# Kernel optimization log

Hardware: AMD Instinct MI355X
Metric: run time of the kernel (lower is better)

Reference implementation:

```python
import jax, jax.numpy as jnp
import numpy as np

H = 16  # num_heads
E = 1024  # embed_dim
HD = E // H  # head_dim = 64


def setup_inputs() -> dict:
    key = jax.random.key(0)
    k1, k2, k3 = jax.random.split(key, 3)
    n, bs = 2048, 2
    # xavier-uniform-ish scale for weights
    seq = jax.random.normal(k1, (n, bs, E), dtype=jnp.float32)
    w_qkv = jax.random.normal(k2, (3 * E, E), dtype=jnp.float32) * (2.0 / (E + 3 * E)) ** 0.5
    b_qkv = jnp.zeros((3 * E,), dtype=jnp.float32)
    w_out = jax.random.normal(k3, (E, E), dtype=jnp.float32) * (1.0 / E) ** 0.5
    b_out = jnp.zeros((E,), dtype=jnp.float32)
    return {"seq": seq, "w_qkv": w_qkv, "b_qkv": b_qkv, "w_out": w_out, "b_out": b_out}


def reference(seq, w_qkv, b_qkv, w_out, b_out):
    n, bs, _ = seq.shape
    # fused QKV projection: [n, bs, 3E]
    qkv = jnp.einsum('nbe,fe->nbf', seq, w_qkv) + b_qkv
    # reshape to [n, bs, 3, H, HD] then split -> q,k,v each [n, bs, H, HD]
    qkv = qkv.reshape(n, bs, 3, H, HD)
    q = qkv[:, :, 0] / jnp.asarray(HD, seq.dtype) ** 0.5
    k = qkv[:, :, 1]
    v = qkv[:, :, 2]
    # scores [bs, H, n, n] -- explicitly materialized as in the original
    attn = jnp.einsum('qbhd,kbhd->bhqk', q, k)
    attn = jax.nn.softmax(attn, axis=-1)
    # weighted values back to [n, bs, H, HD] -> [n, bs, E]
    out = jnp.einsum('bhqk,kbhd->qbhd', attn, v).reshape(n, bs, E)
    out = jnp.einsum('nbe,fe->nbf', out, w_out) + b_out
    return out
```

## Files before the change

### kernel.cpp

```cpp
#include <hip/hip_runtime.h>

typedef unsigned short u16;
typedef unsigned int u32;
typedef __bf16 bf16_8 __attribute__((ext_vector_type(8)));
typedef short s16x8 __attribute__((ext_vector_type(8)));
typedef short s16x4 __attribute__((ext_vector_type(4)));
typedef float f32x4 __attribute__((ext_vector_type(4)));

#define NQ 2048
#define BSZ 2
#define EDIM 1024
#define NH 16
#define HDIM 64
#define MROWS (NQ * BSZ)
#define F3 (3 * EDIM)

__device__ __forceinline__ float bf2f(u16 u) {
  u32 x = ((u32)u) << 16;
  return __builtin_bit_cast(float, x);
}
__device__ __forceinline__ u16 f2bf(float f) {
  u32 x = __builtin_bit_cast(u32, f);
  x += 0x7fff + ((x >> 16) & 1);
  return (u16)(x >> 16);
}
__device__ __forceinline__ void gload16(const u16* g, u16* l) {
  __builtin_amdgcn_global_load_lds(
      (const __attribute__((address_space(1))) void*)g,
      (__attribute__((address_space(3))) void*)l, 16, 0, 0);
}

__global__ __launch_bounds__(256) void cvt_f32_bf16(
    const float* __restrict__ in, u16* __restrict__ out, int n) {
  int i = (blockIdx.x * 256 + threadIdx.x) * 4;
  const int stride = gridDim.x * 256 * 4;
  for (; i < n; i += stride) {
    f32x4 v = *(const f32x4*)&in[i];
    s16x4 o;
    o[0] = (short)f2bf(v[0]);
    o[1] = (short)f2bf(v[1]);
    o[2] = (short)f2bf(v[2]);
    o[3] = (short)f2bf(v[3]);
    *(s16x4*)&out[i] = o;
  }
}

__global__ __launch_bounds__(512, 2) void gemm_qkv(
    const u16* __restrict__ A, const u16* __restrict__ B,
    const float* __restrict__ bias,
    u16* __restrict__ out0, u16* __restrict__ out1, u16* __restrict__ out2) {
  constexpr int K = EDIM;
  __shared__ u16 As[2][256 * 32];
  __shared__ u16 Bs[2][192 * 32];
  const int tid = threadIdx.x;
  const int wid = tid >> 6, lane = tid & 63;
  const int wr = wid >> 2, wc = wid & 3;
  const int row0 = blockIdx.y * 256, col0 = blockIdx.x * 192;
  const int g = lane >> 4, l15 = lane & 15;
  const int lr = tid >> 2, lc8 = (tid & 3) * 8;

  auto STAGE = [&](int buf, int kb) {
    gload16(&A[(size_t)(row0 + lr) * K + kb + lc8], &As[buf][wid * 512]);
    gload16(&A[(size_t)(row0 + 128 + lr) * K + kb + lc8],
            &As[buf][4096 + wid * 512]);
    gload16(&B[(size_t)(col0 + lr) * K + kb + lc8], &Bs[buf][wid * 512]);
    if (tid < 256)
      gload16(&B[(size_t)(col0 + 128 + lr) * K + kb + lc8],
              &Bs[buf][4096 + wid * 512]);
  };

  f32x4 acc[8][3];
#pragma unroll
  for (int m = 0; m < 8; ++m)
#pragma unroll
    for (int n = 0; n < 3; ++n) acc[m][n] = f32x4{0.f, 0.f, 0.f, 0.f};

  STAGE(0, 0);
  __syncthreads();
  int cur = 0;
  for (int t = 0; t < 32; ++t) {
    if (t < 31) STAGE(cur ^ 1, (t + 1) * 32);
    bf16_8 af[8], bf[3];
#pragma unroll
    for (int m = 0; m < 8; ++m)
      af[m] = __builtin_bit_cast(
          bf16_8, *(const s16x8*)&As[cur][(wr * 128 + m * 16 + l15) * 32 + g * 8]);
#pragma unroll
    for (int n = 0; n < 3; ++n)
      bf[n] = __builtin_bit_cast(
          bf16_8, *(const s16x8*)&Bs[cur][(wc * 48 + n * 16 + l15) * 32 + g * 8]);
#pragma unroll
    for (int m = 0; m < 8; ++m)
#pragma unroll
      for (int n = 0; n < 3; ++n)
        acc[m][n] = __builtin_amdgcn_mfma_f32_16x16x32_bf16(af[m], bf[n],
                                                            acc[m][n], 0, 0, 0);
    __syncthreads();
    cur ^= 1;
  }

  const int orow = row0 + wr * 128;
  const int ocol = col0 + wc * 48;
#pragma unroll
  for (int m = 0; m < 8; ++m) {
#pragma unroll
    for (int n = 0; n < 3; ++n) {
      const int f = ocol + n * 16 + l15;
      const float bv = bias[f];
#pragma unroll
      for (int j = 0; j < 4; ++j) {
        const int r = orow + m * 16 + g * 4 + j;
        const float v = acc[m][n][j] + bv;
        const int part = f >> 10, e = f & 1023;
        const int h = e >> 6, d = e & 63;
        const int nq = r >> 1, b = r & 1;
        const int bh = b * NH + h;
        if (part == 0)
          out0[((size_t)bh * NQ + nq) * HDIM + d] = f2bf(v * 0.125f);
        else if (part == 1)
          out1[((size_t)bh * NQ + nq) * HDIM + d] = f2bf(v);
        else
          out2[((size_t)bh * HDIM + d) * NQ + nq] = f2bf(v);
      }
    }
  }
}

__global__ __launch_bounds__(256) void gemm_out(
    const u16* __restrict__ A, const u16* __restrict__ B,
    const float* __restrict__ bias, float* __restrict__ outf) {
  constexpr int K = EDIM;
  __shared__ u16 As[2][128 * 32];
  __shared__ u16 Bs[2][128 * 32];
  const int tid = threadIdx.x;
  const int wid = tid >> 6, lane = tid & 63;
  const int wm = wid >> 1, wn = wid & 1;
  const int row0 = blockIdx.y * 128, col0 = blockIdx.x * 128;
  const int g = lane >> 4, l15 = lane & 15;
  const int lr = tid >> 2, lc8 = (tid & 3) * 8;

  auto STAGE = [&](int buf, int kb) {
#pragma unroll
    for (int s = 0; s < 2; ++s) {
      gload16(&A[(size_t)(row0 + s * 64 + lr) * K + kb + lc8],
              &As[buf][s * 2048 + wid * 512]);
      gload16(&B[(size_t)(col0 + s * 64 + lr) * K + kb + lc8],
              &Bs[buf][s * 2048 + wid * 512]);
    }
  };

  f32x4 acc[4][4];
#pragma unroll
  for (int m = 0; m < 4; ++m)
#pragma unroll
    for (int n = 0; n < 4; ++n) acc[m][n] = f32x4{0.f, 0.f, 0.f, 0.f};

  STAGE(0, 0);
  __syncthreads();
  int cur = 0;
  for (int t = 0; t < 32; ++t) {
    if (t < 31) STAGE(cur ^ 1, (t + 1) * 32);
    bf16_8 af[4], bf[4];
#pragma unroll
    for (int m = 0; m < 4; ++m)
      af[m] = __builtin_bit_cast(
          bf16_8, *(const s16x8*)&As[cur][(wm * 64 + m * 16 + l15) * 32 + g * 8]);
#pragma unroll
    for (int n = 0; n < 4; ++n)
      bf[n] = __builtin_bit_cast(
          bf16_8, *(const s16x8*)&Bs[cur][(wn * 64 + n * 16 + l15) * 32 + g * 8]);
#pragma unroll
    for (int m = 0; m < 4; ++m)
#pragma unroll
      for (int n = 0; n < 4; ++n)
        acc[m][n] = __builtin_amdgcn_mfma_f32_16x16x32_bf16(af[m], bf[n],
                                                            acc[m][n], 0, 0, 0);
    __syncthreads();
    cur ^= 1;
  }

  const int orow = row0 + wm * 64;
  const int ocol = col0 + wn * 64;
#pragma unroll
  for (int m = 0; m < 4; ++m)
#pragma unroll
    for (int n = 0; n < 4; ++n) {
      const int f = ocol + n * 16 + l15;
      const float bv = bias[f];
#pragma unroll
      for (int j = 0; j < 4; ++j)
        outf[(size_t)(orow + m * 16 + g * 4 + j) * EDIM + f] =
            acc[m][n][j] + bv;
    }
}

__global__ __launch_bounds__(256) void attn_split(
    const u16* __restrict__ Qs, const u16* __restrict__ Ks,
    const u16* __restrict__ Vt, u16* __restrict__ op0, u16* __restrict__ op1,
    float* __restrict__ rsp) {
  __shared__ u16 KVs[2][8192];
  __shared__ u16 Pl[4][2][1024];
  const int tid = threadIdx.x;
  const int wid = tid >> 6, lane = tid & 63;
  const int g = lane >> 4, l15 = lane & 15;
  const int bh = blockIdx.y, z = blockIdx.z;
  const int kt0 = z * (NQ / 2);
  const int qrow = blockIdx.x * 128 + wid * 32;
  const int rxor = (l15 >> 1) & 7;
  const int r4 = tid >> 2, c8 = (tid & 3) * 8;

  auto STAGE = [&](int buf, int kt) {
#pragma unroll
    for (int p = 0; p < 2; ++p) {
      gload16(&Ks[((size_t)bh * NQ + kt + r4) * HDIM + p * 32 + c8],
              &KVs[buf][p * 2048 + wid * 512]);
      gload16(&Vt[((size_t)bh * HDIM + r4) * NQ + kt + p * 32 + c8],
              &KVs[buf][4096 + p * 2048 + wid * 512]);
    }
  };

  bf16_8 qf[2][2];
#pragma unroll
  for (int qb = 0; qb < 2; ++qb)
#pragma unroll
    for (int c = 0; c < 2; ++c)
      qf[qb][c] = __builtin_bit_cast(
          bf16_8, *(const s16x8*)&Qs[((size_t)bh * NQ + qrow + qb * 16 + l15) *
                                         HDIM + c * 32 + g * 8]);

  f32x4 oacc[2][4];
#pragma unroll
  for (int qb = 0; qb < 2; ++qb)
#pragma unroll
    for (int n = 0; n < 4; ++n) oacc[qb][n] = f32x4{0.f, 0.f, 0.f, 0.f};
  float rs[2][4] = {{0.f, 0.f, 0.f, 0.f}, {0.f, 0.f, 0.f, 0.f}};

  STAGE(0, kt0);
  __syncthreads();
  int cur = 0;
  for (int t = 0; t < 16; ++t) {
    if (t < 15) STAGE(cur ^ 1, kt0 + (t + 1) * 64);

#pragma unroll
    for (int n = 0; n < 4; ++n) {
      bf16_8 kf0 = __builtin_bit_cast(
          bf16_8, *(const s16x8*)&KVs[cur][(n * 16 + l15) * 32 + g * 8]);
      bf16_8 kf1 = __builtin_bit_cast(
          bf16_8, *(const s16x8*)&KVs[cur][2048 + (n * 16 + l15) * 32 + g * 8]);
      const int chunk = 2 * n + (l15 >> 3), wsub = l15 & 7;
#pragma unroll
      for (int qb = 0; qb < 2; ++qb) {
        f32x4 s = f32x4{0.f, 0.f, 0.f, 0.f};
        s = __builtin_amdgcn_mfma_f32_16x16x32_bf16(qf[qb][0], kf0, s, 0, 0, 0);
        s = __builtin_amdgcn_mfma_f32_16x16x32_bf16(qf[qb][1], kf1, s, 0, 0, 0);
#pragma unroll
        for (int j = 0; j < 4; ++j) {
          float p = __expf(s[j]);
          rs[qb][j] += p;
          const int q = g * 4 + j;
          Pl[wid][qb][q * 64 + ((chunk ^ ((q >> 1) & 7)) << 3) + wsub] = f2bf(p);
        }
      }
    }

#pragma unroll
    for (int n = 0; n < 4; ++n) {
      bf16_8 vf0 = __builtin_bit_cast(
          bf16_8, *(const s16x8*)&KVs[cur][4096 + (n * 16 + l15) * 32 + g * 8]);
      bf16_8 vf1 = __builtin_bit_cast(
          bf16_8, *(const s16x8*)&KVs[cur][6144 + (n * 16 + l15) * 32 + g * 8]);
#pragma unroll
      for (int qb = 0; qb < 2; ++qb) {
        bf16_8 pf0 = __builtin_bit_cast(
            bf16_8, *(const s16x8*)&Pl[wid][qb][l15 * 64 + ((g ^ rxor) << 3)]);
        bf16_8 pf1 = __builtin_bit_cast(
            bf16_8, *(const s16x8*)&Pl[wid][qb][l15 * 64 + (((g + 4) ^ rxor) << 3)]);
        oacc[qb][n] = __builtin_amdgcn_mfma_f32_16x16x32_bf16(pf0, vf0, oacc[qb][n], 0, 0, 0);
        oacc[qb][n] = __builtin_amdgcn_mfma_f32_16x16x32_bf16(pf1, vf1, oacc[qb][n], 0, 0, 0);
      }
    }
    __syncthreads();
    cur ^= 1;
  }

  u16* op = z ? op1 : op0;
  const int b = bh >> 4, h = bh & 15;
#pragma unroll
  for (int qb = 0; qb < 2; ++qb) {
#pragma unroll
    for (int j = 0; j < 4; ++j) {
      float ts = rs[qb][j];
      ts += __shfl_xor(ts, 1);
      ts += __shfl_xor(ts, 2);
      ts += __shfl_xor(ts, 4);
      ts += __shfl_xor(ts, 8);
      if (l15 == 0)
        rsp[(size_t)(z * 32 + bh) * NQ + qrow + qb * 16 + g * 4 + j] = ts;
    }
#pragma unroll
    for (int n = 0; n < 4; ++n)
#pragma unroll
      for (int j = 0; j < 4; ++j) {
        const int q = qrow + qb * 16 + g * 4 + j;
        op[((size_t)q * BSZ + b) * EDIM + h * 64 + n * 16 + l15] =
            f2bf(oacc[qb][n][j]);
      }
  }
}

__global__ __launch_bounds__(256) void attn_combine(
    const u16* __restrict__ p0, const u16* __restrict__ p1,
    const float* __restrict__ rsp, u16* __restrict__ AO) {
  const size_t i8 = (size_t)blockIdx.x * 256 + threadIdx.x;
  const size_t i = i8 * 8;
  const int e = (int)(i & 1023);
  const int b = (int)((i >> 10) & 1);
  const int q = (int)(i >> 11);
  const int bh = b * NH + (e >> 6);
  const float inv = 1.0f / (rsp[(size_t)bh * NQ + q] +
                            rsp[(size_t)(32 + bh) * NQ + q]);
  s16x8 a = *(const s16x8*)&p0[i];
  s16x8 c = *(const s16x8*)&p1[i];
  s16x8 o;
#pragma unroll
  for (int j = 0; j < 8; ++j)
    o[j] = (short)f2bf((bf2f((u16)a[j]) + bf2f((u16)c[j])) * inv);
  *(s16x8*)&AO[i] = o;
}

extern "C" void kernel_launch(void* const* d_in, const int* in_sizes, int n_in,
                              void* d_out, int out_size, void* d_ws,
                              size_t ws_size, hipStream_t stream) {
  const float* seq = (const float*)d_in[0];
  const float* w_qkv = (const float*)d_in[1];
  const float* b_qkv = (const float*)d_in[2];
  const float* w_out = (const float*)d_in[3];
  const float* b_out = (const float*)d_in[4];
  float* out = (float*)d_out;

  const size_t per = (size_t)BSZ * NH * NQ * HDIM;
  u16* Qs = (u16*)d_ws;
  u16* Ks = Qs + per;
  u16* Vt = Ks + per;
  u16* AO = Vt + per;
  u16* seqb = AO + (size_t)MROWS * EDIM;
  u16* wqkvb = seqb + (size_t)MROWS * EDIM;
  u16* woutb = wqkvb + (size_t)F3 * EDIM;
  float* rsp = (float*)wqkvb;

  cvt_f32_bf16<<<1024, 256, 0, stream>>>(seq, seqb, MROWS * EDIM);
  cvt_f32_bf16<<<1024, 256, 0, stream>>>(w_qkv, wqkvb, F3 * EDIM);
  cvt_f32_bf16<<<512, 256, 0, stream>>>(w_out, woutb, EDIM * EDIM);

  gemm_qkv<<<dim3(F3 / 192, MROWS / 256), 512, 0, stream>>>(
      seqb, wqkvb, b_qkv, Qs, Ks, Vt);
  attn_split<<<dim3(NQ / 128, BSZ * NH, 2), 256, 0, stream>>>(
      Qs, Ks, Vt, AO, seqb, rsp);
  attn_combine<<<(MROWS * EDIM) / (256 * 8), 256, 0, stream>>>(
      AO, seqb, rsp, AO);
  gemm_out<<<dim3(EDIM / 128, MROWS / 128), 256, 0, stream>>>(
      AO, woutb, b_out, out);
}
```

Before: 235.7 us.

## Unify QKV and output GEMMs into templated 128x128 kernel, use exp2 softmax

```diff
diff --git a/kernel.cpp b/kernel.cpp
--- a/kernel.cpp
+++ b/kernel.cpp
@@ -14,6 +14,14 @@
 #define HDIM 64
 #define MROWS (NQ * BSZ)
 #define F3 (3 * EDIM)
+
+#define QSCALE 0.1803368801f
+
+#if defined(__HIP_DEVICE_COMPILE__) && __has_builtin(__builtin_amdgcn_exp2f)
+#define EXP2F(x) __builtin_amdgcn_exp2f(x)
+#else
+#define EXP2F(x) exp2f(x)
+#endif
 
 __device__ __forceinline__ float bf2f(u16 u) {
   u32 x = ((u32)u) << 16;
@@ -45,90 +53,12 @@
   }
 }
 
-__global__ __launch_bounds__(512, 2) void gemm_qkv(
+template <int MODE>
+__global__ __launch_bounds__(256) void gemm_bt(
     const u16* __restrict__ A, const u16* __restrict__ B,
     const float* __restrict__ bias,
-    u16* __restrict__ out0, u16* __restrict__ out1, u16* __restrict__ out2) {
-  constexpr int K = EDIM;
-  __shared__ u16 As[2][256 * 32];
-  __shared__ u16 Bs[2][192 * 32];
-  const int tid = threadIdx.x;
-  const int wid = tid >> 6, lane = tid & 63;
-  const int wr = wid >> 2, wc = wid & 3;
-  const int row0 = blockIdx.y * 256, col0 = blockIdx.x * 192;
-  const int g = lane >> 4, l15 = lane & 15;
-  const int lr = tid >> 2, lc8 = (tid & 3) * 8;
-
-  auto STAGE = [&](int buf, int kb) {
-    gload16(&A[(size_t)(row0 + lr) * K + kb + lc8], &As[buf][wid * 512]);
-    gload16(&A[(size_t)(row0 + 128 + lr) * K + kb + lc8],
-            &As[buf][4096 + wid * 512]);
-    gload16(&B[(size_t)(col0 + lr) * K + kb + lc8], &Bs[buf][wid * 512]);
-    if (tid < 256)
-      gload16(&B[(size_t)(col0 + 128 + lr) * K + kb + lc8],
-              &Bs[buf][4096 + wid * 512]);
-  };
-
-  f32x4 acc[8][3];
-#pragma unroll
-  for (int m = 0; m < 8; ++m)
-#pragma unroll
-    for (int n = 0; n < 3; ++n) acc[m][n] = f32x4{0.f, 0.f, 0.f, 0.f};
-
-  STAGE(0, 0);
-  __syncthreads();
-  int cur = 0;
-  for (int t = 0; t < 32; ++t) {
-    if (t < 31) STAGE(cur ^ 1, (t + 1) * 32);
-    bf16_8 af[8], bf[3];
-#pragma unroll
-    for (int m = 0; m < 8; ++m)
-      af[m] = __builtin_bit_cast(
-          bf16_8, *(const s16x8*)&As[cur][(wr * 128 + m * 16 + l15) * 32 + g * 8]);
-#pragma unroll
-    for (int n = 0; n < 3; ++n)
-      bf[n] = __builtin_bit_cast(
-          bf16_8, *(const s16x8*)&Bs[cur][(wc * 48 + n * 16 + l15) * 32 + g * 8]);
-#pragma unroll
-    for (int m = 0; m < 8; ++m)
-#pragma unroll
-      for (int n = 0; n < 3; ++n)
-        acc[m][n] = __builtin_amdgcn_mfma_f32_16x16x32_bf16(af[m], bf[n],
-                                                            acc[m][n], 0, 0, 0);
-    __syncthreads();
-    cur ^= 1;
-  }
-
-  const int orow = row0 + wr * 128;
-  const int ocol = col0 + wc * 48;
-#pragma unroll
-  for (int m = 0; m < 8; ++m) {
-#pragma unroll
-    for (int n = 0; n < 3; ++n) {
-      const int f = ocol + n * 16 + l15;
-      const float bv = bias[f];
-#pragma unroll
-      for (int j = 0; j < 4; ++j) {
-        const int r = orow + m * 16 + g * 4 + j;
-        const float v = acc[m][n][j] + bv;
-        const int part = f >> 10, e = f & 1023;
-        const int h = e >> 6, d = e & 63;
-        const int nq = r >> 1, b = r & 1;
-        const int bh = b * NH + h;
-        if (part == 0)
-          out0[((size_t)bh * NQ + nq) * HDIM + d] = f2bf(v * 0.125f);
-        else if (part == 1)
-          out1[((size_t)bh * NQ + nq) * HDIM + d] = f2bf(v);
-        else
-          out2[((size_t)bh * HDIM + d) * NQ + nq] = f2bf(v);
-      }
-    }
-  }
-}
-
-__global__ __launch_bounds__(256) void gemm_out(
-    const u16* __restrict__ A, const u16* __restrict__ B,
-    const float* __restrict__ bias, float* __restrict__ outf) {
+    u16* __restrict__ out0, u16* __restrict__ out1, u16* __restrict__ out2,
+    float* __restrict__ outf) {
   constexpr int K = EDIM;
   __shared__ u16 As[2][128 * 32];
   __shared__ u16 Bs[2][128 * 32];
@@ -182,16 +112,32 @@
   const int orow = row0 + wm * 64;
   const int ocol = col0 + wn * 64;
 #pragma unroll
-  for (int m = 0; m < 4; ++m)
+  for (int m = 0; m < 4; ++m) {
 #pragma unroll
     for (int n = 0; n < 4; ++n) {
       const int f = ocol + n * 16 + l15;
       const float bv = bias[f];
 #pragma unroll
-      for (int j = 0; j < 4; ++j)
-        outf[(size_t)(orow + m * 16 + g * 4 + j) * EDIM + f] =
-            acc[m][n][j] + bv;
-    }
+      for (int j = 0; j < 4; ++j) {
+        const int r = orow + m * 16 + g * 4 + j;
+        const float v = acc[m][n][j] + bv;
+        if (MODE == 0) {
+          const int part = f >> 10, e = f & 1023;
+          const int h = e >> 6, d = e & 63;
+          const int nq = r >> 1, b = r & 1;
+          const int bh = b * NH + h;
+          if (part == 0)
+            out0[((size_t)bh * NQ + nq) * HDIM + d] = f2bf(v * QSCALE);
+          else if (part == 1)
+            out1[((size_t)bh * NQ + nq) * HDIM + d] = f2bf(v);
+          else
+            out2[((size_t)bh * HDIM + d) * NQ + nq] = f2bf(v);
+        } else {
+          outf[(size_t)r * EDIM + f] = v;
+        }
+      }
+    }
+  }
 }
 
 __global__ __launch_bounds__(256) void attn_split(
@@ -199,7 +145,7 @@
     const u16* __restrict__ Vt, u16* __restrict__ op0, u16* __restrict__ op1,
     float* __restrict__ rsp) {
   __shared__ u16 KVs[2][8192];
-  __shared__ u16 Pl[4][2][1024];
+  __shared__ u16 Pl[4][1024];
   const int tid = threadIdx.x;
   const int wid = tid >> 6, lane = tid & 63;
   const int g = lane >> 4, l15 = lane & 15;
@@ -242,39 +188,35 @@
     if (t < 15) STAGE(cur ^ 1, kt0 + (t + 1) * 64);
 
 #pragma unroll
-    for (int n = 0; n < 4; ++n) {
-      bf16_8 kf0 = __builtin_bit_cast(
-          bf16_8, *(const s16x8*)&KVs[cur][(n * 16 + l15) * 32 + g * 8]);
-      bf16_8 kf1 = __builtin_bit_cast(
-          bf16_8, *(const s16x8*)&KVs[cur][2048 + (n * 16 + l15) * 32 + g * 8]);
-      const int chunk = 2 * n + (l15 >> 3), wsub = l15 & 7;
-#pragma unroll
-      for (int qb = 0; qb < 2; ++qb) {
+    for (int qb = 0; qb < 2; ++qb) {
+#pragma unroll
+      for (int n = 0; n < 4; ++n) {
+        bf16_8 kf0 = __builtin_bit_cast(
+            bf16_8, *(const s16x8*)&KVs[cur][(n * 16 + l15) * 32 + g * 8]);
+        bf16_8 kf1 = __builtin_bit_cast(
+            bf16_8, *(const s16x8*)&KVs[cur][2048 + (n * 16 + l15) * 32 + g * 8]);
+        const int chunk = 2 * n + (l15 >> 3), wsub = l15 & 7;
         f32x4 s = f32x4{0.f, 0.f, 0.f, 0.f};
         s = __builtin_amdgcn_mfma_f32_16x16x32_bf16(qf[qb][0], kf0, s, 0, 0, 0);
         s = __builtin_amdgcn_mfma_f32_16x16x32_bf16(qf[qb][1], kf1, s, 0, 0, 0);
 #pragma unroll
         for (int j = 0; j < 4; ++j) {
-          float p = __expf(s[j]);
+          float p = EXP2F(s[j]);
           rs[qb][j] += p;
           const int q = g * 4 + j;
-          Pl[wid][qb][q * 64 + ((chunk ^ ((q >> 1) & 7)) << 3) + wsub] = f2bf(p);
+          Pl[wid][q * 64 + ((chunk ^ ((q >> 1) & 7)) << 3) + wsub] = f2bf(p);
         }
       }
-    }
-
-#pragma unroll
-    for (int n = 0; n < 4; ++n) {
-      bf16_8 vf0 = __builtin_bit_cast(
-          bf16_8, *(const s16x8*)&KVs[cur][4096 + (n * 16 + l15) * 32 + g * 8]);
-      bf16_8 vf1 = __builtin_bit_cast(
-          bf16_8, *(const s16x8*)&KVs[cur][6144 + (n * 16 + l15) * 32 + g * 8]);
-#pragma unroll
-      for (int qb = 0; qb < 2; ++qb) {
+#pragma unroll
+      for (int n = 0; n < 4; ++n) {
+        bf16_8 vf0 = __builtin_bit_cast(
+            bf16_8, *(const s16x8*)&KVs[cur][4096 + (n * 16 + l15) * 32 + g * 8]);
+        bf16_8 vf1 = __builtin_bit_cast(
+            bf16_8, *(const s16x8*)&KVs[cur][6144 + (n * 16 + l15) * 32 + g * 8]);
         bf16_8 pf0 = __builtin_bit_cast(
-            bf16_8, *(const s16x8*)&Pl[wid][qb][l15 * 64 + ((g ^ rxor) << 3)]);
+            bf16_8, *(const s16x8*)&Pl[wid][l15 * 64 + ((g ^ rxor) << 3)]);
         bf16_8 pf1 = __builtin_bit_cast(
-            bf16_8, *(const s16x8*)&Pl[wid][qb][l15 * 64 + (((g + 4) ^ rxor) << 3)]);
+            bf16_8, *(const s16x8*)&Pl[wid][l15 * 64 + (((g + 4) ^ rxor) << 3)]);
         oacc[qb][n] = __builtin_amdgcn_mfma_f32_16x16x32_bf16(pf0, vf0, oacc[qb][n], 0, 0, 0);
         oacc[qb][n] = __builtin_amdgcn_mfma_f32_16x16x32_bf16(pf1, vf1, oacc[qb][n], 0, 0, 0);
       }
@@ -352,12 +294,12 @@
   cvt_f32_bf16<<<1024, 256, 0, stream>>>(w_qkv, wqkvb, F3 * EDIM);
   cvt_f32_bf16<<<512, 256, 0, stream>>>(w_out, woutb, EDIM * EDIM);
 
-  gemm_qkv<<<dim3(F3 / 192, MROWS / 256), 512, 0, stream>>>(
-      seqb, wqkvb, b_qkv, Qs, Ks, Vt);
+  gemm_bt<0><<<dim3(F3 / 128, MROWS / 128), 256, 0, stream>>>(
+      seqb, wqkvb, b_qkv, Qs, Ks, Vt, nullptr);
   attn_split<<<dim3(NQ / 128, BSZ * NH, 2), 256, 0, stream>>>(
       Qs, Ks, Vt, AO, seqb, rsp);
   attn_combine<<<(MROWS * EDIM) / (256 * 8), 256, 0, stream>>>(
       AO, seqb, rsp, AO);
-  gemm_out<<<dim3(EDIM / 128, MROWS / 128), 256, 0, stream>>>(
-      AO, woutb, b_out, out);
-}
+  gemm_bt<1><<<dim3(EDIM / 128, MROWS / 128), 256, 0, stream>>>(
+      AO, woutb, b_out, nullptr, nullptr, nullptr, out);
+}
```

Result: faster. 223.7 us (-5.1%).
